# Kernel tuning notes

Measured on AMD Instinct MI355X. Metric: run time of the kernel, lower is better.

The kernel has to match this reference:

```python
import jax, jax.numpy as jnp
import numpy as np

H = 8            # num_heads
DK = 256         # head_qk_dim
DV = 512         # head_v_dim
EPS = 1e-5
ROPE_BASE = 10000.0


def _rope(x):
    # x: [B, T, H, DK]; GPT-NeoX style (non-interleaved halves), seqlen_offset=0
    B, T, h, d = x.shape
    inv_freq = 1.0 / (ROPE_BASE ** (jnp.arange(0, d, 2, dtype=jnp.float32) / d))  # [d/2]
    t = jnp.arange(T, dtype=jnp.float32)
    freqs = t[:, None] * inv_freq[None, :]              # [T, d/2]
    cos = jnp.cos(freqs)[None, :, None, :]              # [1, T, 1, d/2]
    sin = jnp.sin(freqs)[None, :, None, :]
    x1, x2 = x[..., : d // 2], x[..., d // 2 :]
    return jnp.concatenate([x1 * cos - x2 * sin, x2 * cos + x1 * sin], axis=-1)


def setup_inputs() -> dict:
    key = jax.random.key(0)
    ks = jax.random.split(key, 7)
    hidden = 2048
    B, T = 2, 2048
    w = 0.02
    return {
        "hidden_states": jax.random.normal(ks[0], (B, T, hidden), jnp.float32),
        "Wq": jax.random.normal(ks[1], (hidden, H * DK), jnp.float32) * w,
        "Wk": jax.random.normal(ks[2], (hidden, H * DK), jnp.float32) * w,
        "Wv": jax.random.normal(ks[3], (hidden, H * DV), jnp.float32) * w,
        "Wg": jax.random.normal(ks[4], (hidden, H * DV), jnp.float32) * w,
        "Wo": jax.random.normal(ks[5], (H * DV, hidden), jnp.float32) * w,
        "g_norm_weight": jnp.ones((DV,), jnp.float32),
    }


def reference(hidden_states, Wq, Wk, Wv, Wg, Wo, g_norm_weight):
    B, T, _ = hidden_states.shape
    q = (hidden_states @ Wq).reshape(B, T, H, DK)
    k = (hidden_states @ Wk).reshape(B, T, H, DK)
    v = (hidden_states @ Wv).reshape(B, T, H, DV)
    g = (hidden_states @ Wg).reshape(B, T, H, DV)

    q = _rope(q)
    k = _rope(k)

    # per-head RetNet decay: gamma_h = 1 - 2^(-5-h)
    gamma = 1.0 - jnp.exp2(-5.0 - jnp.arange(H, dtype=jnp.float32))     # [H]
    idx = jnp.arange(T)
    diff = idx[:, None] - idx[None, :]                                   # [T, T]
    causal = diff >= 0
    log2g = jnp.log2(gamma)[:, None, None]                               # [H,1,1]
    D = jnp.where(causal[None], jnp.exp2(log2g * jnp.where(causal, diff, 0)[None]), 0.0)  # [H,T,T]

    scale = DK ** -0.5
    scores = jnp.einsum("bihd,bjhd->bhij", q * scale, k) * D[None]       # [B,H,T,T]
    o = jnp.einsum("bhij,bjhd->bihd", scores, v)                          # [B,T,H,DV]

    # fused RMSNorm (per head over DV) + swish gate
    rms = jax.lax.rsqrt(jnp.mean(o * o, axis=-1, keepdims=True) + EPS)
    o = o * rms * g_norm_weight
    o = o * (g * jax.nn.sigmoid(g))

    return o.reshape(B, T, H * DV) @ Wo
```

## Files before the change

kernel.cpp:

```cpp
#include <hip/hip_runtime.h>
#include <hip/hip_bf16.h>
#include <math.h>

#define NH 8
#define DKk 256
#define DVv 512
#define Bn 2
#define Tn 2048
#define HID 2048
#define EPSf 1e-5f

typedef __bf16 bf16x8 __attribute__((ext_vector_type(8)));
typedef float f32x4 __attribute__((ext_vector_type(4)));
typedef unsigned short us8 __attribute__((ext_vector_type(8)));
using bf16 = __hip_bfloat16;
typedef unsigned short ushort_t;

__device__ __forceinline__ void gload_lds16(const void* g, void* lds_base) {
  __builtin_amdgcn_global_load_lds(
      (const __attribute__((address_space(1))) void*)g,
      (__attribute__((address_space(3))) void*)lds_base, 16, 0, 0);
}

__device__ __forceinline__ ushort_t f2bf_raw(float f) {
  bf16 h = __float2bfloat16(f);
  return *reinterpret_cast<ushort_t*>(&h);
}
__device__ __forceinline__ float bf2f_raw(ushort_t u) {
  union { unsigned int i; float f; } v; v.i = ((unsigned int)u) << 16; return v.f;
}

__global__ void k_f32_to_bf16(const float4* __restrict__ in, ushort4* __restrict__ out, int n4) {
  int i = blockIdx.x * blockDim.x + threadIdx.x;
  if (i >= n4) return;
  float4 v = in[i];
  ushort4 o;
  o.x = f2bf_raw(v.x); o.y = f2bf_raw(v.y); o.z = f2bf_raw(v.z); o.w = f2bf_raw(v.w);
  out[i] = o;
}

__global__ void k_transpose_w(const float* __restrict__ W, bf16* __restrict__ WT, int K, int N) {
  __shared__ float t[32][33];
  int n0 = blockIdx.x * 32, k0 = blockIdx.y * 32;
  int tx = threadIdx.x, ty = threadIdx.y;
#pragma unroll
  for (int i = 0; i < 4; i++)
    t[ty + i * 8][tx] = W[(size_t)(k0 + ty + i * 8) * N + n0 + tx];
  __syncthreads();
#pragma unroll
  for (int i = 0; i < 4; i++)
    WT[(size_t)(n0 + ty + i * 8) * K + k0 + tx] = __float2bfloat16(t[tx][ty + i * 8]);
}

__global__ void k_build_vS(const ushort_t* __restrict__ v, ushort_t* __restrict__ vS) {
  __shared__ ushort_t t[32 * 520];
  const int tid = threadIdx.x;
  const int kt = blockIdx.x;
  const int bh = blockIdx.y;
  const int b = bh >> 3, h = bh & 7;
#pragma unroll
  for (int r = 0; r < 8; r++) {
    int j = r * 4 + (tid >> 6);
    int vec = tid & 63;
    us8 d = *(const us8*)(v + (((size_t)(b * Tn + kt * 32 + j) * NH + h) * DVv) + vec * 8);
    *(us8*)(&t[j * 520 + vec * 8]) = d;
  }
  __syncthreads();
#pragma unroll
  for (int u = 0; u < 8; u++) {
    int uid = u * 256 + tid;
    int chunk = uid >> 9;
    int dv = uid & 511;
    us8 o;
#pragma unroll
    for (int jj = 0; jj < 8; jj++) o[jj] = t[(chunk * 8 + jj) * 520 + dv];
    *(us8*)(vS + ((size_t)(bh * 64 + kt) * 2048 + chunk * 512 + dv) * 8) = o;
  }
}

__global__ void k_rope(bf16* __restrict__ x, float scale) {
  int tid = blockIdx.x * 256 + threadIdx.x;
  int i = tid & 127;
  int h = (tid >> 7) & 7;
  int t = (tid >> 10) & (Tn - 1);
  int b = tid >> 21;
  float inv = exp2f(-(float)i * (13.287712379549449f / 128.0f));
  float ang = (float)t * inv;
  float s, c;
  sincosf(ang, &s, &c);
  size_t base = ((size_t)(b * Tn + t) * NH + h) * DKk + i;
  float x1 = __bfloat162float(x[base]);
  float x2 = __bfloat162float(x[base + 128]);
  x[base]       = __float2bfloat16((x1 * c - x2 * s) * scale);
  x[base + 128] = __float2bfloat16((x2 * c + x1 * s) * scale);
}

template <bool OUT_BF16>
__global__ __launch_bounds__(256) void k_gemm(const bf16* __restrict__ A, const bf16* __restrict__ BT,
                                              void* __restrict__ Cout, int M, int N, int K) {
  __shared__ __align__(16) bf16 a_lds[128 * 32];
  __shared__ __align__(16) bf16 b_lds[128 * 32];
  const int tid = threadIdx.x;
  const int l = tid & 63;
  const int w = tid >> 6;
  const int wr = w >> 1, wc = w & 1;
  const int bid = blockIdx.y * gridDim.x + blockIdx.x;
  const int cpx = (gridDim.x * gridDim.y) >> 3;
  const int s = (bid & 7) * cpx + (bid >> 3);
  const int bx = s / gridDim.y, by = s % gridDim.y;
  const int m0 = by * 128, n0 = bx * 128;
  const int quad = l >> 4, c16 = l & 15;

  const int lrow = l >> 2;
  const int loff = (l & 3) * 16;
  const char* aG0 = (const char*)(A + (size_t)(m0 + w * 32 + lrow) * K) + loff;
  const char* aG1 = (const char*)(A + (size_t)(m0 + w * 32 + 16 + lrow) * K) + loff;
  const char* bG0 = (const char*)(BT + (size_t)(n0 + w * 32 + lrow) * K) + loff;
  const char* bG1 = (const char*)(BT + (size_t)(n0 + w * 32 + 16 + lrow) * K) + loff;
  char* aL0 = (char*)a_lds + w * 2048;
  char* aL1 = (char*)a_lds + w * 2048 + 1024;
  char* bL0 = (char*)b_lds + w * 2048;
  char* bL1 = (char*)b_lds + w * 2048 + 1024;

  f32x4 acc[4][4];
  const f32x4 fz = {0.f, 0.f, 0.f, 0.f};
#pragma unroll
  for (int r = 0; r < 4; r++)
#pragma unroll
    for (int c = 0; c < 4; c++) acc[r][c] = fz;

  for (int k0 = 0; k0 < K; k0 += 32) {
    __syncthreads();
    size_t kb = (size_t)k0 * 2;
    gload_lds16(aG0 + kb, aL0);
    gload_lds16(aG1 + kb, aL1);
    gload_lds16(bG0 + kb, bL0);
    gload_lds16(bG1 + kb, bL1);
    __syncthreads();
    bf16x8 af[4], bfv[4];
#pragma unroll
    for (int r = 0; r < 4; r++)
      af[r] = *(const bf16x8*)(a_lds + (wr * 64 + r * 16 + c16) * 32 + quad * 8);
#pragma unroll
    for (int c = 0; c < 4; c++)
      bfv[c] = *(const bf16x8*)(b_lds + (wc * 64 + c * 16 + c16) * 32 + quad * 8);
#pragma unroll
    for (int r = 0; r < 4; r++)
#pragma unroll
      for (int c = 0; c < 4; c++)
        acc[r][c] = __builtin_amdgcn_mfma_f32_16x16x32_bf16(af[r], bfv[c], acc[r][c], 0, 0, 0);
  }

#pragma unroll
  for (int r = 0; r < 4; r++)
#pragma unroll
    for (int c = 0; c < 4; c++)
#pragma unroll
      for (int rr = 0; rr < 4; rr++) {
        int m = m0 + wr * 64 + r * 16 + quad * 4 + rr;
        int n = n0 + wc * 64 + c * 16 + c16;
        float val = acc[r][c][rr];
        if (OUT_BF16) ((bf16*)Cout)[(size_t)m * N + n] = __float2bfloat16(val);
        else          ((float*)Cout)[(size_t)m * N + n] = val;
      }
}

#define BARX() asm volatile("s_barrier" ::: "memory")
#define LGKM0() { asm volatile("s_waitcnt lgkmcnt(0)" ::: "memory"); __builtin_amdgcn_sched_barrier(0); }
#define VMW8() asm volatile("s_waitcnt vmcnt(8)" ::: "memory")
#define VMW0() asm volatile("s_waitcnt vmcnt(0)" ::: "memory")
#define PRIO1 __builtin_amdgcn_s_setprio(1)
#define PRIO0 __builtin_amdgcn_s_setprio(0)

#define QUADX(MH, NHh)                                                             \
  { _Pragma("unroll") for (int kk_ = 0; kk_ < 2; ++kk_)                            \
    _Pragma("unroll") for (int mf_ = 0; mf_ < 4; ++mf_)                            \
    _Pragma("unroll") for (int nf_ = 0; nf_ < 2; ++nf_)                            \
      acc[(MH)*4 + mf_][(NHh)*2 + nf_] = __builtin_amdgcn_mfma_f32_16x16x32_bf16(  \
          ar[(MH)*4 + mf_][kk_], br[(NHh)*2 + nf_][kk_],                           \
          acc[(MH)*4 + mf_][(NHh)*2 + nf_], 0, 0, 0); }

__global__ __launch_bounds__(512, 2) void k_gemm8(const bf16* __restrict__ A, const bf16* __restrict__ BT,
                                                  bf16* __restrict__ O0, bf16* __restrict__ O1,
                                                  int nsplit, int M, int Ntot, int K) {
  extern __shared__ char lds[];
  const int tid = threadIdx.x;
  const int lane = tid & 63;
  const int w = tid >> 6;
  const int wr = w >> 2;
  const int wc = w & 3;
  const int quad = lane >> 4, c16 = lane & 15;
  const int bid = blockIdx.y * gridDim.x + blockIdx.x;
  const int cpx = (gridDim.x * gridDim.y) >> 3;
  const int sw = (bid & 7) * cpx + (bid >> 3);
  const int bx = sw / gridDim.y, by = sw % gridDim.y;
  const int m0 = by * 256, n0 = bx * 256;

  const int srow = (w << 4) | (lane >> 3);
  const int gsw = (((lane & 7) ^ (lane >> 3)) << 4);
  const size_t rowBytes = (size_t)K * 2;
  const char* aS = (const char*)(A + (size_t)(m0 + srow) * K) + gsw;
  const char* bS = (const char*)(BT + (size_t)(n0 + srow) * K) + gsw;

  auto stage = [&](int matB, int buf, int h, int t) {
    const char* base = (matB ? bS : aS) + (size_t)h * 128 * rowBytes + (size_t)t * 128;
    char* ldst = lds + buf * 65536 + matB * 32768 + h * 16384 + w * 2048;
    gload_lds16(base, ldst);
    gload_lds16(base + 8 * rowBytes, ldst + 1024);
  };
  auto ldA = [&](int buf, int mf, int kk) -> bf16x8 {
    int row = wr * 128 + mf * 16 + c16;
    return *(const bf16x8*)(lds + buf * 65536 + row * 128 + ((((kk << 2) | quad) ^ (c16 & 7)) << 4));
  };
  auto ldB = [&](int buf, int nf, int kk) -> bf16x8 {
    int row = wc * 64 + nf * 16 + c16;
    return *(const bf16x8*)(lds + buf * 65536 + 32768 + row * 128 + ((((kk << 2) | quad) ^ (c16 & 7)) << 4));
  };

  f32x4 acc[8][4];
  const f32x4 fz = {0.f, 0.f, 0.f, 0.f};
#pragma unroll
  for (int i = 0; i < 8; i++)
#pragma unroll
    for (int j = 0; j < 4; j++) acc[i][j] = fz;
  bf16x8 ar[8][2], br[4][2];

  const int nT = K >> 6;
  const int nIter = nT >> 1;

  stage(0, 0, 0, 0); stage(0, 0, 1, 0);
  stage(1, 0, 0, 0); stage(1, 0, 1, 0);
  stage(0, 1, 0, 1); stage(0, 1, 1, 1);
  stage(1, 1, 0, 1); stage(1, 1, 1, 1);
  VMW8();
  BARX();

  for (int it = 0; it < nIter; ++it) {
    const int t = it * 2;
    const bool last = (it == nIter - 1);
#pragma unroll
    for (int mf = 0; mf < 4; ++mf) { ar[mf][0] = ldA(0, mf, 0); ar[mf][1] = ldA(0, mf, 1); }
#pragma unroll
    for (int nf = 0; nf < 2; ++nf) { br[nf][0] = ldB(0, nf, 0); br[nf][1] = ldB(0, nf, 1); }
    BARX(); LGKM0();
    PRIO1; QUADX(0, 0); PRIO0;
    BARX();
#pragma unroll
    for (int mf = 4; mf < 8; ++mf) { ar[mf][0] = ldA(0, mf, 0); ar[mf][1] = ldA(0, mf, 1); }
#pragma unroll
    for (int nf = 2; nf < 4; ++nf) { br[nf][0] = ldB(0, nf, 0); br[nf][1] = ldB(0, nf, 1); }
    BARX(); LGKM0();
    PRIO1; QUADX(0, 1); PRIO0;
    BARX();
    if (!last) { stage(0, 0, 0, t + 2); stage(0, 0, 1, t + 2); }
    BARX();
    PRIO1; QUADX(1, 0); PRIO0;
    BARX();
    if (!last) { stage(1, 0, 0, t + 2); stage(1, 0, 1, t + 2); }
    BARX();
    PRIO1; QUADX(1, 1); PRIO0;
    if (!last) { VMW8(); } else { VMW0(); }
    BARX();
#pragma unroll
    for (int mf = 0; mf < 4; ++mf) { ar[mf][0] = ldA(1, mf, 0); ar[mf][1] = ldA(1, mf, 1); }
#pragma unroll
    for (int nf = 0; nf < 2; ++nf) { br[nf][0] = ldB(1, nf, 0); br[nf][1] = ldB(1, nf, 1); }
    BARX(); LGKM0();
    PRIO1; QUADX(0, 0); PRIO0;
    BARX();
#pragma unroll
    for (int mf = 4; mf < 8; ++mf) { ar[mf][0] = ldA(1, mf, 0); ar[mf][1] = ldA(1, mf, 1); }
#pragma unroll
    for (int nf = 2; nf < 4; ++nf) { br[nf][0] = ldB(1, nf, 0); br[nf][1] = ldB(1, nf, 1); }
    BARX(); LGKM0();
    PRIO1; QUADX(0, 1); PRIO0;
    BARX();
    if (!last) { stage(0, 1, 0, t + 3); stage(0, 1, 1, t + 3); }
    BARX();
    PRIO1; QUADX(1, 0); PRIO0;
    BARX();
    if (!last) { stage(1, 1, 0, t + 3); stage(1, 1, 1, t + 3); }
    BARX();
    PRIO1; QUADX(1, 1); PRIO0;
    if (!last) VMW8();
    BARX();
  }

  bf16* Ob; int ldo, nc0;
  if (n0 < nsplit) { Ob = O0; ldo = nsplit; nc0 = n0; }
  else             { Ob = O1; ldo = Ntot - nsplit; nc0 = n0 - nsplit; }
#pragma unroll
  for (int mf = 0; mf < 8; ++mf)
#pragma unroll
    for (int nf = 0; nf < 4; ++nf)
#pragma unroll
      for (int rr = 0; rr < 4; ++rr) {
        int m = m0 + wr * 128 + mf * 16 + quad * 4 + rr;
        int n = nc0 + wc * 64 + nf * 16 + c16;
        Ob[(size_t)m * ldo + n] = __float2bfloat16(acc[mf][nf][rr]);
      }
}

__global__ __launch_bounds__(256, 1) void k_retention(const bf16* __restrict__ q, const bf16* __restrict__ k,
                                                      const char* __restrict__ vS, const bf16* __restrict__ g,
                                                      const float* __restrict__ gnw, bf16* __restrict__ X) {
  extern __shared__ char smem[];
  ushort_t* p_lds = (ushort_t*)(smem + 98304);
  float* red = (float*)(smem + 103424);
  bf16* o_lds = (bf16*)smem;

  const int tid = threadIdx.x;
  const int l = tid & 63, w = tid >> 6;
  const int quad = l >> 4, c16 = l & 15;

  const int bid = blockIdx.x;
  const int qt = 31 - (bid >> 4);
  const int bh = bid & 15;
  const int b = bh >> 3, h = bh & 7;
  const int q0 = qt * 64;

  bf16x8 qf[8];
  {
    const bf16* qrow = q + ((size_t)(b * Tn + q0 + w * 16 + c16) * NH + h) * DKk + quad * 8;
#pragma unroll
    for (int c = 0; c < 8; c++) qf[c] = *(const bf16x8*)(qrow + c * 32);
  }

  const float log2g = log2f(1.0f - exp2f(-5.0f - (float)h));

  f32x4 acc[4][8];
  const f32x4 fz = {0.f, 0.f, 0.f, 0.f};
#pragma unroll
  for (int rt = 0; rt < 4; rt++)
#pragma unroll
    for (int n = 0; n < 8; n++) acc[rt][n] = fz;

  const int ktmax = 2 * qt + 1;
  const float Dcut = 30.0f / (-log2g);
  int kt0 = (int)fmaxf(0.0f, floorf(((float)q0 - Dcut) * (1.0f / 32.0f)));

  const char* vS_tilebase = vS + (size_t)(bh * 64) * 32768;

  auto stageKV = [&](int kt, int pbuf) {
#pragma unroll
    for (int i = 0; i < 4; i++) {
      int instr = w * 4 + i;
      int j = instr * 2 + (l >> 5);
      int cg = (l & 31) ^ (j & 7);
      const char* gp = (const char*)(k + ((size_t)(b * Tn + kt * 32 + j) * NH + h) * DKk) + cg * 16;
      gload_lds16(gp, smem + pbuf * 16384 + instr * 1024);
    }
#pragma unroll
    for (int i = 0; i < 8; i++) {
      int instr = w * 8 + i;
      const char* gp = vS_tilebase + (size_t)kt * 32768 + instr * 1024 + l * 16;
      gload_lds16(gp, smem + 32768 + pbuf * 32768 + instr * 1024);
    }
  };

  stageKV(kt0, 0);

  for (int kt = kt0; kt <= ktmax; kt++) {
    const int pb = (kt - kt0) & 1;
    if (kt < ktmax) {
      stageKV(kt + 1, pb ^ 1);
      asm volatile("s_waitcnt vmcnt(12)" ::: "memory");
    } else {
      asm volatile("s_waitcnt vmcnt(0)" ::: "memory");
    }
    __builtin_amdgcn_sched_barrier(0);
    __builtin_amdgcn_s_barrier();

    f32x4 sacc[2] = {fz, fz};
#pragma unroll
    for (int jt = 0; jt < 2; jt++)
#pragma unroll
      for (int c = 0; c < 8; c++) {
        const char* kp = smem + pb * 16384 + (jt * 16 + c16) * 512 + (((c * 4 + quad) ^ (c16 & 7)) * 16);
        bf16x8 bfrag = *(const bf16x8*)kp;
        sacc[jt] = __builtin_amdgcn_mfma_f32_16x16x32_bf16(qf[c], bfrag, sacc[jt], 0, 0, 0);
      }

#pragma unroll
    for (int jt = 0; jt < 2; jt++)
#pragma unroll
      for (int r = 0; r < 4; r++) {
        int ig = q0 + w * 16 + quad * 4 + r;
        int jg = kt * 32 + jt * 16 + c16;
        int d = ig - jg;
        float val = (d >= 0) ? sacc[jt][r] * exp2f(log2g * (float)d) : 0.0f;
        p_lds[(w * 16 + quad * 4 + r) * 40 + jt * 16 + c16] = f2bf_raw(val);
      }
    asm volatile("s_waitcnt lgkmcnt(0)" ::: "memory");
    __builtin_amdgcn_sched_barrier(0);
    __builtin_amdgcn_s_barrier();

    bf16x8 pa[4];
#pragma unroll
    for (int rt = 0; rt < 4; rt++)
      pa[rt] = *(const bf16x8*)((const char*)p_lds + (rt * 16 + c16) * 80 + quad * 16);
    const char* v_lds = smem + 32768 + pb * 32768;
#pragma unroll
    for (int n = 0; n < 8; n++) {
      bf16x8 bv = *(const bf16x8*)(v_lds + quad * 8192 + (w * 128 + n * 16 + c16) * 16);
#pragma unroll
      for (int rt = 0; rt < 4; rt++)
        acc[rt][n] = __builtin_amdgcn_mfma_f32_16x16x32_bf16(pa[rt], bv, acc[rt][n], 0, 0, 0);
    }
    asm volatile("s_waitcnt lgkmcnt(0)" ::: "memory");
    __builtin_amdgcn_sched_barrier(0);
    __builtin_amdgcn_s_barrier();
  }

  __syncthreads();
#pragma unroll
  for (int rt = 0; rt < 4; rt++)
#pragma unroll
    for (int r = 0; r < 4; r++) {
      float s = 0.f;
#pragma unroll
      for (int n = 0; n < 8; n++) { float v = acc[rt][n][r]; s += v * v; }
      s += __shfl_xor(s, 1);
      s += __shfl_xor(s, 2);
      s += __shfl_xor(s, 4);
      s += __shfl_xor(s, 8);
      if (c16 == 0) red[(rt * 16 + quad * 4 + r) * 4 + w] = s;
    }
  __syncthreads();
  float ss[4][4];
#pragma unroll
  for (int rt = 0; rt < 4; rt++)
#pragma unroll
    for (int r = 0; r < 4; r++) {
      int row = rt * 16 + quad * 4 + r;
      float tot = red[row * 4] + red[row * 4 + 1] + red[row * 4 + 2] + red[row * 4 + 3];
      ss[rt][r] = rsqrtf(tot * (1.0f / DVv) + EPSf);
    }
  __syncthreads();

#pragma unroll
  for (int n = 0; n < 8; n++) {
    int col = w * 128 + n * 16 + c16;
    float gw = gnw[col];
#pragma unroll
    for (int rt = 0; rt < 4; rt++)
#pragma unroll
      for (int r = 0; r < 4; r++) {
        int row = rt * 16 + quad * 4 + r;
        o_lds[row * 512 + col] = __float2bfloat16(acc[rt][n][r] * ss[rt][r] * gw);
      }
  }
  __syncthreads();

#pragma unroll
  for (int it = 0; it < 16; it++) {
    int cid = it * 256 + tid;
    int row = cid >> 6;
    int cp = (cid & 63) * 8;
    const ushort_t* gp = (const ushort_t*)g + ((size_t)(b * Tn + q0 + row) * NH + h) * DVv + cp;
    us8 gv = *(const us8*)gp;
    us8 ov;
#pragma unroll
    for (int e = 0; e < 8; e++) {
      float gf = bf2f_raw(gv[e]);
      float gate = gf / (1.0f + expf(-gf));
      float of = __bfloat162float(o_lds[row * 512 + cp + e]);
      ov[e] = f2bf_raw(of * gate);
    }
    *(us8*)((ushort_t*)X + ((size_t)(b * Tn + q0 + row) * NH + h) * DVv + cp) = ov;
  }
}

extern "C" void kernel_launch(void* const* d_in, const int* in_sizes, int n_in,
                              void* d_out, int out_size, void* d_ws, size_t ws_size,
                              hipStream_t stream) {
  const float* hs  = (const float*)d_in[0];
  const float* Wq  = (const float*)d_in[1];
  const float* Wk  = (const float*)d_in[2];
  const float* Wv  = (const float*)d_in[3];
  const float* Wg  = (const float*)d_in[4];
  const float* Wo  = (const float*)d_in[5];
  const float* gnw = (const float*)d_in[6];
  float* out = (float*)d_out;
  char* ws = (char*)d_ws;

  bf16* hsb = (bf16*)(ws);
  bf16* WqT = (bf16*)(ws + 16777216);
  bf16* WkT = (bf16*)(ws + 25165824);
  bf16* WvT = (bf16*)(ws + 33554432);
  bf16* WgT = (bf16*)(ws + 50331648);
  char* vSb = ws;
  bf16* WoT = (bf16*)(ws + 33554432);
  bf16* qb = (bf16*)(ws + 67108864);
  bf16* kb = (bf16*)(ws + 83886080);
  bf16* vb = (bf16*)(ws + 100663296);
  bf16* gb = (bf16*)(ws + 134217728);
  bf16* Xb = vb;

  static bool attr_done = false;
  if (!attr_done) {
    hipFuncSetAttribute((const void*)k_gemm8, hipFuncAttributeMaxDynamicSharedMemorySize, 131072);
    hipFuncSetAttribute((const void*)k_retention, hipFuncAttributeMaxDynamicSharedMemorySize, 104448);
    attr_done = true;
  }

  dim3 tb(32, 8);

  k_f32_to_bf16<<<8192, 256, 0, stream>>>((const float4*)hs, (ushort4*)hsb, 2097152);
  k_transpose_w<<<dim3(HID / 32, HID / 32), tb, 0, stream>>>(Wq, WqT, HID, HID);
  k_transpose_w<<<dim3(HID / 32, HID / 32), tb, 0, stream>>>(Wk, WkT, HID, HID);
  k_transpose_w<<<dim3(NH * DVv / 32, HID / 32), tb, 0, stream>>>(Wv, WvT, HID, NH * DVv);
  k_transpose_w<<<dim3(NH * DVv / 32, HID / 32), tb, 0, stream>>>(Wg, WgT, HID, NH * DVv);
  k_gemm8<<<dim3(16, 16), 512, 131072, stream>>>(hsb, WqT, qb, kb, 2048, 4096, 4096, 2048);
  k_gemm8<<<dim3(32, 16), 512, 131072, stream>>>(hsb, WvT, vb, gb, 4096, 4096, 8192, 2048);
  k_rope<<<16384, 256, 0, stream>>>(qb, 0.0625f);
  k_rope<<<16384, 256, 0, stream>>>(kb, 1.0f);
  k_build_vS<<<dim3(64, 16), 256, 0, stream>>>((const ushort_t*)vb, (ushort_t*)vSb);
  k_transpose_w<<<dim3(HID / 32, NH * DVv / 32), tb, 0, stream>>>(Wo, WoT, NH * DVv, HID);
  k_retention<<<512, 256, 104448, stream>>>(qb, kb, vSb, gb, gnw, Xb);
  k_gemm<false><<<dim3(16, 32), 256, 0, stream>>>(Xb, WoT, out, 4096, 2048, 4096);
}
```

Measured before the change: 676.8 us.

## Restructure retention pipeline to single V buffer for two blocks per CU

The retention kernel now stages K and V separately with a single V buffer and double-buffered P tiles, cutting LDS from about 102KB to 75KB so two blocks can share a CU (launch bounds raised to 2). The loop is re-pipelined so the S computation for tile kt overlaps the K prefetch, while PV for the previous tile runs before V is restaged. Query-tile ordering is changed to pair long and short causal rows across the two halves of the grid for load balance. Separately, the block-index swizzle in both GEMM kernels is removed in favour of plain row-major tile mapping, which may change L2 locality. The tradeoff is less V prefetch overlap and more barriers per iteration.

```diff
diff --git a/kernel.cpp b/kernel.cpp
--- a/kernel.cpp
+++ b/kernel.cpp
@@ -104,11 +104,7 @@
   const int l = tid & 63;
   const int w = tid >> 6;
   const int wr = w >> 1, wc = w & 1;
-  const int bid = blockIdx.y * gridDim.x + blockIdx.x;
-  const int cpx = (gridDim.x * gridDim.y) >> 3;
-  const int s = (bid & 7) * cpx + (bid >> 3);
-  const int bx = s / gridDim.y, by = s % gridDim.y;
-  const int m0 = by * 128, n0 = bx * 128;
+  const int m0 = blockIdx.y * 128, n0 = blockIdx.x * 128;
   const int quad = l >> 4, c16 = l & 15;
 
   const int lrow = l >> 2;
@@ -190,11 +186,7 @@
   const int wr = w >> 2;
   const int wc = w & 3;
   const int quad = lane >> 4, c16 = lane & 15;
-  const int bid = blockIdx.y * gridDim.x + blockIdx.x;
-  const int cpx = (gridDim.x * gridDim.y) >> 3;
-  const int sw = (bid & 7) * cpx + (bid >> 3);
-  const int bx = sw / gridDim.y, by = sw % gridDim.y;
-  const int m0 = by * 256, n0 = bx * 256;
+  const int m0 = blockIdx.y * 256, n0 = blockIdx.x * 256;
 
   const int srow = (w << 4) | (lane >> 3);
   const int gsw = (((lane & 7) ^ (lane >> 3)) << 4);
@@ -301,12 +293,11 @@
       }
 }
 
-__global__ __launch_bounds__(256, 1) void k_retention(const bf16* __restrict__ q, const bf16* __restrict__ k,
+__global__ __launch_bounds__(256, 2) void k_retention(const bf16* __restrict__ q, const bf16* __restrict__ k,
                                                       const char* __restrict__ vS, const bf16* __restrict__ g,
                                                       const float* __restrict__ gnw, bf16* __restrict__ X) {
   extern __shared__ char smem[];
-  ushort_t* p_lds = (ushort_t*)(smem + 98304);
-  float* red = (float*)(smem + 103424);
+  float* red = (float*)(smem + 75776);
   bf16* o_lds = (bf16*)smem;
 
   const int tid = threadIdx.x;
@@ -314,7 +305,8 @@
   const int quad = l >> 4, c16 = l & 15;
 
   const int bid = blockIdx.x;
-  const int qt = 31 - (bid >> 4);
+  const int u = (bid & 255) >> 4;
+  const int qt = (bid < 256) ? (31 - u) : u;
   const int bh = bid & 15;
   const int b = bh >> 3, h = bh & 7;
   const int q0 = qt * 64;
@@ -341,36 +333,33 @@
 
   const char* vS_tilebase = vS + (size_t)(bh * 64) * 32768;
 
-  auto stageKV = [&](int kt, int pbuf) {
+  auto stageK = [&](int kt) {
+    const int pb = (kt - kt0) & 1;
+#pragma unroll
+    for (int i = 0; i < 1; i++) {
+      int instr = w * 4;
+      (void)instr;
+    }
 #pragma unroll
     for (int i = 0; i < 4; i++) {
       int instr = w * 4 + i;
       int j = instr * 2 + (l >> 5);
       int cg = (l & 31) ^ (j & 7);
       const char* gp = (const char*)(k + ((size_t)(b * Tn + kt * 32 + j) * NH + h) * DKk) + cg * 16;
-      gload_lds16(gp, smem + pbuf * 16384 + instr * 1024);
-    }
+      gload_lds16(gp, smem + pb * 16384 + instr * 1024);
+    }
+  };
+  auto stageV = [&](int kt) {
 #pragma unroll
     for (int i = 0; i < 8; i++) {
       int instr = w * 8 + i;
       const char* gp = vS_tilebase + (size_t)kt * 32768 + instr * 1024 + l * 16;
-      gload_lds16(gp, smem + 32768 + pbuf * 32768 + instr * 1024);
-    }
-  };
-
-  stageKV(kt0, 0);
-
-  for (int kt = kt0; kt <= ktmax; kt++) {
+      gload_lds16(gp, smem + 32768 + instr * 1024);
+    }
+  };
+
+  auto S_phase = [&](int kt) {
     const int pb = (kt - kt0) & 1;
-    if (kt < ktmax) {
-      stageKV(kt + 1, pb ^ 1);
-      asm volatile("s_waitcnt vmcnt(12)" ::: "memory");
-    } else {
-      asm volatile("s_waitcnt vmcnt(0)" ::: "memory");
-    }
-    __builtin_amdgcn_sched_barrier(0);
-    __builtin_amdgcn_s_barrier();
-
     f32x4 sacc[2] = {fz, fz};
 #pragma unroll
     for (int jt = 0; jt < 2; jt++)
@@ -380,7 +369,7 @@
         bf16x8 bfrag = *(const bf16x8*)kp;
         sacc[jt] = __builtin_amdgcn_mfma_f32_16x16x32_bf16(qf[c], bfrag, sacc[jt], 0, 0, 0);
       }
-
+    ushort_t* pbuf = (ushort_t*)(smem + 65536 + pb * 5120);
 #pragma unroll
     for (int jt = 0; jt < 2; jt++)
 #pragma unroll
@@ -389,17 +378,18 @@
         int jg = kt * 32 + jt * 16 + c16;
         int d = ig - jg;
         float val = (d >= 0) ? sacc[jt][r] * exp2f(log2g * (float)d) : 0.0f;
-        p_lds[(w * 16 + quad * 4 + r) * 40 + jt * 16 + c16] = f2bf_raw(val);
+        pbuf[(w * 16 + quad * 4 + r) * 40 + jt * 16 + c16] = f2bf_raw(val);
       }
-    asm volatile("s_waitcnt lgkmcnt(0)" ::: "memory");
-    __builtin_amdgcn_sched_barrier(0);
-    __builtin_amdgcn_s_barrier();
-
+  };
+
+  auto PV_phase = [&](int kt) {
+    const int pb = (kt - kt0) & 1;
+    const char* pbuf = smem + 65536 + pb * 5120;
     bf16x8 pa[4];
 #pragma unroll
     for (int rt = 0; rt < 4; rt++)
-      pa[rt] = *(const bf16x8*)((const char*)p_lds + (rt * 16 + c16) * 80 + quad * 16);
-    const char* v_lds = smem + 32768 + pb * 32768;
+      pa[rt] = *(const bf16x8*)(pbuf + (rt * 16 + c16) * 80 + quad * 16);
+    const char* v_lds = smem + 32768;
 #pragma unroll
     for (int n = 0; n < 8; n++) {
       bf16x8 bv = *(const bf16x8*)(v_lds + quad * 8192 + (w * 128 + n * 16 + c16) * 16);
@@ -407,10 +397,35 @@
       for (int rt = 0; rt < 4; rt++)
         acc[rt][n] = __builtin_amdgcn_mfma_f32_16x16x32_bf16(pa[rt], bv, acc[rt][n], 0, 0, 0);
     }
-    asm volatile("s_waitcnt lgkmcnt(0)" ::: "memory");
-    __builtin_amdgcn_sched_barrier(0);
-    __builtin_amdgcn_s_barrier();
-  }
+  };
+
+#define SBAR() { __builtin_amdgcn_sched_barrier(0); __builtin_amdgcn_s_barrier(); }
+#define WLGKM0() { asm volatile("s_waitcnt lgkmcnt(0)" ::: "memory"); }
+
+  stageK(kt0);
+  stageV(kt0);
+  asm volatile("s_waitcnt vmcnt(8)" ::: "memory");
+  SBAR();
+  S_phase(kt0);
+  if (kt0 + 1 <= ktmax) stageK(kt0 + 1);
+  WLGKM0(); SBAR();
+
+  for (int kt = kt0 + 1; kt <= ktmax; ++kt) {
+    asm volatile("s_waitcnt vmcnt(4)" ::: "memory");
+    SBAR();
+    PV_phase(kt - 1);
+    WLGKM0(); SBAR();
+    stageV(kt);
+    asm volatile("s_waitcnt vmcnt(8)" ::: "memory");
+    SBAR();
+    S_phase(kt);
+    if (kt + 1 <= ktmax) stageK(kt + 1);
+    WLGKM0(); SBAR();
+  }
+
+  asm volatile("s_waitcnt vmcnt(0)" ::: "memory");
+  SBAR();
+  PV_phase(ktmax);
 
   __syncthreads();
 #pragma unroll
@@ -500,7 +515,7 @@
   static bool attr_done = false;
   if (!attr_done) {
     hipFuncSetAttribute((const void*)k_gemm8, hipFuncAttributeMaxDynamicSharedMemorySize, 131072);
-    hipFuncSetAttribute((const void*)k_retention, hipFuncAttributeMaxDynamicSharedMemorySize, 104448);
+    hipFuncSetAttribute((const void*)k_retention, hipFuncAttributeMaxDynamicSharedMemorySize, 76800);
     attr_done = true;
   }
 
@@ -517,6 +532,6 @@
   k_rope<<<16384, 256, 0, stream>>>(kb, 1.0f);
   k_build_vS<<<dim3(64, 16), 256, 0, stream>>>((const ushort_t*)vb, (ushort_t*)vSb);
   k_transpose_w<<<dim3(HID / 32, NH * DVv / 32), tb, 0, stream>>>(Wo, WoT, NH * DVv, HID);
-  k_retention<<<512, 256, 104448, stream>>>(qb, kb, vSb, gb, gnw, Xb);
+  k_retention<<<512, 256, 76800, stream>>>(qb, kb, vSb, gb, gnw, Xb);
   k_gemm<false><<<dim3(16, 32), 256, 0, stream>>>(Xb, WoT, out, 4096, 2048, 4096);
 }
```

New measurement: 645.5 us. 1.05x faster.
